# Kernel tuning notes

Hardware: AMD Instinct MI355X
Metric: run time of the kernel (lower is better)

## Reference

```python
import jax, jax.numpy as jnp
import numpy as np

EPS = 1e-5


def _ln(x, g, b):
    mu = jnp.mean(x, axis=-1, keepdims=True)
    var = jnp.var(x, axis=-1, keepdims=True)
    return (x - mu) * jax.lax.rsqrt(var + EPS) * g + b


def setup_inputs() -> dict:
    key = jax.random.key(0)
    ks = jax.random.split(key, 24)
    B, S, SD, PD, AD = 2, 512, 512, 128, 64
    H = PD * 2
    s = 0.02
    inp = {
        "sequence_input": jax.random.normal(ks[0], (B, S, SD), jnp.float32),
        "pair_input": jax.random.normal(ks[1], (B, S // 2, S // 2, PD), jnp.float32),
        # SequenceToPairBlock params
        "sn_g": jnp.ones((SD,), jnp.float32),
        "sn_b": jnp.zeros((SD,), jnp.float32),
        "Wq": jax.random.normal(ks[2], (SD, PD), jnp.float32) * s,
        "Wk": jax.random.normal(ks[3], (SD, PD), jnp.float32) * s,
        "Wyq": jax.random.normal(ks[4], (SD, PD), jnp.float32) * s,
        "Wyk": jax.random.normal(ks[5], (SD, PD), jnp.float32) * s,
        "Wdist": jax.random.normal(ks[6], (3, PD), jnp.float32) * s,
        "Wout": jax.random.normal(ks[7], (PD, PD), jnp.float32) * s,
        "bout": jnp.zeros((PD,), jnp.float32),
        # RowAttentionBlock params
        "rn_g": jnp.ones((PD,), jnp.float32),
        "rn_b": jnp.zeros((PD,), jnp.float32),
        "Wrq": jax.random.normal(ks[8], (PD, AD), jnp.float32) * s,
        "Wrk": jax.random.normal(ks[9], (PD, AD), jnp.float32) * s,
        "Wrv": jax.random.normal(ks[10], (PD, AD), jnp.float32) * s,
        "brv": jnp.zeros((AD,), jnp.float32),
        "Wro": jax.random.normal(ks[11], (AD, PD), jnp.float32) * s,
        "bro": jnp.zeros((PD,), jnp.float32),
        # PairMLPBlock params
        "mn_g": jnp.ones((PD,), jnp.float32),
        "mn_b": jnp.zeros((PD,), jnp.float32),
        "W1": jax.random.normal(ks[12], (PD, H), jnp.float32) * s,
        "b1": jnp.zeros((H,), jnp.float32),
        "W2": jax.random.normal(ks[13], (H, PD), jnp.float32) * s,
        "b2": jnp.zeros((PD,), jnp.float32),
    }
    return inp


def reference(sequence_input, pair_input, sn_g, sn_b, Wq, Wk, Wyq, Wyk, Wdist, Wout, bout,
              rn_g, rn_b, Wrq, Wrk, Wrv, brv, Wro, bro, mn_g, mn_b, W1, b1, W2, b2):
    # ---- SequenceToPairBlock ----
    x = _ln(sequence_input, sn_g, sn_b)               # [B,S,SD]
    B, S, SD = x.shape
    x = x.reshape(B, S // 2, 2, SD).mean(axis=2)       # avg_pool1d k=2,s=2 (S even) -> [B,P,SD]
    P = x.shape[1]
    q = x @ Wq                                         # [B,P,PD]
    k = x @ Wk
    pair_qk = q[:, :, None, :] + k[:, None, :, :]      # [B,P,P,PD]
    idx = jnp.arange(P, dtype=x.dtype)
    dist = idx[:, None] - idx[None, :]
    dist_scale = jnp.abs(dist) / max(1.0, float(P - 1))
    dist_feats = jnp.stack([dist_scale, jnp.sign(dist), jnp.exp(-dist_scale)], axis=-1)  # [P,P,3]
    pair_dist = dist_feats @ Wdist                     # [P,P,PD], broadcast over batch
    gx = jax.nn.gelu(x, approximate=False)
    yq = gx @ Wyq
    yk = gx @ Wyk
    pair_outer = yq[:, :, None, :] + yk[:, None, :, :]
    y = (pair_qk + pair_dist[None] + pair_outer) @ Wout + bout  # [B,P,P,PD]

    x = pair_input + y

    # ---- RowAttentionBlock (dropout off / eval) ----
    yn = _ln(x, rn_g, rn_b)
    qa = yn @ Wrq                                      # [B,P,P,AD]
    ka = yn @ Wrk
    va = yn @ Wrv + brv
    scale = 1.0 / jnp.sqrt(jnp.asarray(qa.shape[-1], x.dtype))
    logits = jnp.einsum('bird,bisd->birs', qa, ka) * scale
    attn = jax.nn.softmax(logits, axis=-1)
    o = jnp.einsum('birs,bisd->bird', attn, va)
    x = x + (o @ Wro + bro)

    # ---- PairMLPBlock ----
    h = _ln(x, mn_g, mn_b)
    x = x + (jax.nn.relu(h @ W1 + b1) @ W2 + b2)
    return x
```

## Files before the change

### kernel.cpp

```cpp
#include <hip/hip_runtime.h>
#include <hip/hip_bf16.h>

using bf16 = __hip_bfloat16;
typedef unsigned int uint;
typedef unsigned short ushort;
typedef __attribute__((ext_vector_type(8))) short bf16x8;
typedef __attribute__((ext_vector_type(4))) float f32x4;


__device__ __forceinline__ float bfraw(uint u) { return __uint_as_float(u << 16); }
__device__ __forceinline__ ushort f2bf(float f) {
    bf16 h = __float2bfloat16(f);
    return *reinterpret_cast<ushort*>(&h);
}
__device__ __forceinline__ float lbf(ushort u) { return __uint_as_float(((uint)u) << 16); }

#define MFMA_B16(a, b, c) __builtin_amdgcn_mfma_f32_16x16x32_bf16((a), (b), (c), 0, 0, 0)
#define LGKM0() asm volatile("s_waitcnt lgkmcnt(0)" ::: "memory")

__global__ __launch_bounds__(256) void k_ln_pool(
    const float* __restrict__ seq, const float* __restrict__ g,
    const float* __restrict__ be, float* __restrict__ x2)
{
    __shared__ float red[4][4];
    int bp = blockIdx.x;
    int t  = threadIdx.x;
    const float* r0 = seq + (size_t)(bp * 2) * 512;
    const float* r1 = r0 + 512;

    float a0 = r0[t], a1 = r0[t + 256];
    float c0 = r1[t], c1 = r1[t + 256];

    float s0 = a0 + a1, q0 = a0 * a0 + a1 * a1;
    float s1 = c0 + c1, q1 = c0 * c0 + c1 * c1;
#pragma unroll
    for (int off = 32; off; off >>= 1) {
        s0 += __shfl_xor(s0, off); q0 += __shfl_xor(q0, off);
        s1 += __shfl_xor(s1, off); q1 += __shfl_xor(q1, off);
    }
    int w = t >> 6, l = t & 63;
    if (l == 0) { red[0][w] = s0; red[1][w] = q0; red[2][w] = s1; red[3][w] = q1; }
    __syncthreads();
    s0 = red[0][0] + red[0][1] + red[0][2] + red[0][3];
    q0 = red[1][0] + red[1][1] + red[1][2] + red[1][3];
    s1 = red[2][0] + red[2][1] + red[2][2] + red[2][3];
    q1 = red[3][0] + red[3][1] + red[3][2] + red[3][3];

    const float inv = 1.0f / 512.0f;
    float mu0 = s0 * inv, var0 = q0 * inv - mu0 * mu0, rs0 = rsqrtf(var0 + 1e-5f);
    float mu1 = s1 * inv, var1 = q1 * inv - mu1 * mu1, rs1 = rsqrtf(var1 + 1e-5f);

    float g0 = g[t], g1 = g[t + 256];
    float e0 = be[t], e1 = be[t + 256];

    float o0 = 0.5f * ((a0 - mu0) * rs0 * g0 + e0 + (c0 - mu1) * rs1 * g0 + e0);
    float o1 = 0.5f * ((a1 - mu0) * rs0 * g1 + e1 + (c1 - mu1) * rs1 * g1 + e1);

    float* xo = x2 + (size_t)bp * 512;
    xo[t] = o0; xo[t + 256] = o1;
}

__global__ __launch_bounds__(128) void k_proj(
    const float* __restrict__ x2,
    const float* __restrict__ Wq, const float* __restrict__ Wk,
    const float* __restrict__ Wyq, const float* __restrict__ Wyk,
    const float* __restrict__ Wout, const float* __restrict__ bout,
    float* __restrict__ a2, float* __restrict__ c2)
{
    __shared__ float xr[512], gxr[512], ar[128], cr[128];
    int row = blockIdx.x;
    int t   = threadIdx.x;

    for (int u = t; u < 512; u += 128) {
        float v = x2[(size_t)row * 512 + u];
        xr[u]  = v;
        gxr[u] = 0.5f * v * (1.0f + erff(v * 0.70710678118654752f));
    }
    __syncthreads();

    float a = 0.f, c = 0.f;
    for (int s = 0; s < 512; s++) {
        float xs = xr[s], gs = gxr[s];
        a += xs * Wq[s * 128 + t] + gs * Wyq[s * 128 + t];
        c += xs * Wk[s * 128 + t] + gs * Wyk[s * 128 + t];
    }
    ar[t] = a; cr[t] = c;
    __syncthreads();

    float A = bout[t], C = 0.f;
    for (int u = 0; u < 128; u++) {
        float wv = Wout[u * 128 + t];
        A += ar[u] * wv;
        C += cr[u] * wv;
    }
    a2[(size_t)row * 128 + t] = A;
    c2[(size_t)row * 128 + t] = C;
}

__global__ __launch_bounds__(128) void k_wd2(
    const float* __restrict__ Wdist, const float* __restrict__ Wout,
    float* __restrict__ wd2)
{
    int t = threadIdx.x;
#pragma unroll
    for (int f = 0; f < 3; f++) {
        float acc = 0.f;
        for (int u = 0; u < 128; u++)
            acc += Wdist[f * 128 + u] * Wout[u * 128 + t];
        wd2[f * 128 + t] = acc;
    }
}

__global__ __launch_bounds__(512) void k_wt(
    const float* __restrict__ Wrq, const float* __restrict__ Wrk,
    const float* __restrict__ Wrv, const float* __restrict__ Wro,
    ushort* __restrict__ wqF, ushort* __restrict__ wkF,
    ushort* __restrict__ wvF, ushort* __restrict__ wroF)
{
    int idx = blockIdx.x * 512 + threadIdx.x;
    int m = idx >> 13;
    int o = idx & 8191;
    int f = o >> 9;
    int l = (o >> 3) & 63;
    int j = o & 7;
    if (m < 3) {
        int nt = f >> 2, kf = f & 3;
        const float* W = (m == 0) ? Wrq : (m == 1) ? Wrk : Wrv;
        ushort* T = (m == 0) ? wqF : (m == 1) ? wkF : wvF;
        T[o] = f2bf(W[(32 * kf + 8 * (l >> 4) + j) * 64 + 16 * nt + (l & 15)]);
    } else {
        int nt = f >> 1, kf2 = f & 1;
        wroF[o] = f2bf(Wro[(32 * kf2 + 8 * (l >> 4) + j) * 128 + 16 * nt + (l & 15)]);
    }
}

__global__ __launch_bounds__(512) void k_wt12(
    const float* __restrict__ W1, const float* __restrict__ W2,
    ushort* __restrict__ w1F, ushort* __restrict__ w2F)
{
    int idx = blockIdx.x * 512 + threadIdx.x;
    int o = idx & 32767;
    int f = o >> 9;
    int l = (o >> 3) & 63;
    int j = o & 7;
    int kb = f >> 5, nt = (f >> 2) & 7, kf = f & 3;
    if (idx < 32768) {
        int R = 128 * kb + 16 * nt + (l & 15);
        int C = 32 * kf + 8 * (l >> 4) + j;
        w1F[o] = f2bf(W1[C * 256 + R]);
    } else {
        int R2 = 16 * nt + (l & 15);
        int C2 = 128 * kb + 32 * kf + 8 * (l >> 4) + j;
        w2F[o] = f2bf(W2[C2 * 128 + R2]);
    }
}

__global__ __launch_bounds__(256) void k_assemble(
    const float* __restrict__ pair, const float* __restrict__ a2,
    const float* __restrict__ c2, const float* __restrict__ wd2,
    float* __restrict__ xout)
{
    size_t idx = (size_t)blockIdx.x * 256 + threadIdx.x;
    int d = (int)(idx & 127);
    size_t r = idx >> 7;
    int j = (int)(r & 255); r >>= 8;
    int i = (int)(r & 255);
    int b = (int)(r >> 8);

    float ds = fabsf((float)(i - j)) * (1.0f / 255.0f);
    float sg = (float)((i > j) - (i < j));
    float ex = __expf(-ds);

    float v = pair[idx]
            + a2[(size_t)(b * 256 + i) * 128 + d]
            + c2[(size_t)(b * 256 + j) * 128 + d]
            + ds * wd2[d] + sg * wd2[128 + d] + ex * wd2[256 + d];
    xout[idx] = v;
}

__global__ __launch_bounds__(64, 2) void k_qkv_asm(
    float* __restrict__ x, const float* __restrict__ pair,
    const float* __restrict__ a2, const float* __restrict__ c2,
    const float* __restrict__ wd2,
    const float* __restrict__ rn_g, const float* __restrict__ rn_b,
    const ushort* __restrict__ wqF, const ushort* __restrict__ wkF,
    const ushort* __restrict__ wvF, const float* __restrict__ brv,
    ushort* __restrict__ qA, ushort* __restrict__ kB, ushort* __restrict__ vB)
{
    __shared__ __align__(16) unsigned char smem[12288];
    int l = threadIdx.x;
    int g = l >> 4, lr = l & 15;
    int s = blockIdx.x & 511;
    int c = blockIdx.x >> 9;
    size_t xbase = (size_t)s * 32768 + (size_t)(32 * c) * 128;

    {
        float gl0 = rn_g[l], gl1 = rn_g[l + 64];
        float el0 = rn_b[l], el1 = rn_b[l + 64];
        int b  = s >> 8;
        int ii = s & 255;
        float a20 = a2[(size_t)s * 128 + l];
        float a21 = a2[(size_t)s * 128 + l + 64];
        float wdA0 = wd2[l],       wdA1 = wd2[l + 64];
        float wdB0 = wd2[128 + l], wdB1 = wd2[128 + l + 64];
        float wdC0 = wd2[256 + l], wdC1 = wd2[256 + l + 64];
#pragma unroll
        for (int bb = 0; bb < 8; bb++) {
            float p0[4], p1[4], c20[4], c21[4];
#pragma unroll
            for (int rr = 0; rr < 4; rr++) {
                size_t ro = xbase + (size_t)(4 * bb + rr) * 128;
                p0[rr] = pair[ro + l]; p1[rr] = pair[ro + l + 64];
                int j = 32 * c + 4 * bb + rr;
                c20[rr] = c2[(size_t)(b * 256 + j) * 128 + l];
                c21[rr] = c2[(size_t)(b * 256 + j) * 128 + l + 64];
            }
#pragma unroll
            for (int rr = 0; rr < 4; rr++) {
                int rloc = 4 * bb + rr;
                int j = 32 * c + rloc;
                float dsv = fabsf((float)(ii - j)) * (1.0f / 255.0f);
                float sgv = (float)((ii > j) - (ii < j));
                float exv = __expf(-dsv);
                float x0 = p0[rr] + a20 + c20[rr] + dsv * wdA0 + sgv * wdB0 + exv * wdC0;
                float x1 = p1[rr] + a21 + c21[rr] + dsv * wdA1 + sgv * wdB1 + exv * wdC1;
                size_t ro = xbase + (size_t)rloc * 128;
                x[ro + l] = x0; x[ro + l + 64] = x1;
                float sS = x0 + x1, qS = x0 * x0 + x1 * x1;
#pragma unroll
                for (int off = 32; off; off >>= 1) { sS += __shfl_xor(sS, off); qS += __shfl_xor(qS, off); }
                float mu = sS * (1.0f / 128.0f);
                float var = qS * (1.0f / 128.0f) - mu * mu;
                float rs = rsqrtf(var + 1e-5f);
                int sw = (rloc & 7) << 4;
                *(ushort*)(smem + rloc * 256 + ((2 * l) ^ sw))        = f2bf((x0 - mu) * rs * gl0 + el0);
                *(ushort*)(smem + rloc * 256 + ((2 * (l + 64)) ^ sw)) = f2bf((x1 - mu) * rs * gl1 + el1);
            }
        }
    }
    LGKM0();

    bf16x8 afr[2][4];
#pragma unroll
    for (int mt = 0; mt < 2; mt++)
#pragma unroll
        for (int kf = 0; kf < 4; kf++) {
            int row = 16 * mt + lr;
            afr[mt][kf] = *(const bf16x8*)(smem + row * 256 + ((16 * g + 64 * kf) ^ ((row & 7) << 4)));
        }

    unsigned char* dscr = smem + 8192;

#pragma unroll
    for (int mqk = 0; mqk < 2; mqk++) {
        const ushort* wF = mqk ? wkF : wqF;
        ushort* dst = mqk ? kB : qA;
        float scale = mqk ? 1.0f : 0.125f;
#pragma unroll
        for (int mt = 0; mt < 2; mt++) {
#pragma unroll
            for (int nt = 0; nt < 4; nt++) {
                f32x4 acc = (f32x4){0.f, 0.f, 0.f, 0.f};
#pragma unroll
                for (int kf = 0; kf < 4; kf++) {
                    bf16x8 bfr = *(const bf16x8*)(wF + (((nt << 2) | kf) << 9) + (l << 3));
                    acc = MFMA_B16(afr[mt][kf], bfr, acc);
                }
                int col = lr + 16 * nt;
#pragma unroll
                for (int i = 0; i < 4; i++) {
                    int row = 4 * g + i + 16 * mt;
                    int ad = row * 128 + ((2 * col) ^ ((row & 7) << 4));
                    *(ushort*)(dscr + ad) = f2bf(acc[i] * scale);
                }
            }
        }
        LGKM0();
#pragma unroll
        for (int mt = 0; mt < 2; mt++)
#pragma unroll
            for (int kf2 = 0; kf2 < 2; kf2++) {
                int row = 16 * mt + lr;
                int rd = row * 128 + ((64 * kf2 + 16 * g) ^ ((row & 7) << 4));
                bf16x8 v = *(const bf16x8*)(dscr + rd);
                *(bf16x8*)(dst + ((size_t)((s * 16 + 2 * c + mt) * 2 + kf2) << 9) + (l << 3)) = v;
            }
        LGKM0();
    }

#pragma unroll
    for (int mt = 0; mt < 2; mt++) {
#pragma unroll
        for (int nt = 0; nt < 4; nt++) {
            f32x4 acc = (f32x4){0.f, 0.f, 0.f, 0.f};
#pragma unroll
            for (int kf = 0; kf < 4; kf++) {
                bf16x8 bfr = *(const bf16x8*)(wvF + (((nt << 2) | kf) << 9) + (l << 3));
                acc = MFMA_B16(afr[mt][kf], bfr, acc);
            }
            int d = lr + 16 * nt;
            float bv = brv[d];
#pragma unroll
            for (int i = 0; i < 4; i++) {
                int kk = 4 * g + i + 16 * mt;
                int ad = d * 64 + ((2 * kk) ^ ((d & 3) << 4));
                *(ushort*)(dscr + ad) = f2bf(acc[i] + bv);
            }
        }
    }
    LGKM0();
#pragma unroll
    for (int nt2 = 0; nt2 < 4; nt2++) {
        int d = 16 * nt2 + lr;
        int rd = d * 64 + ((16 * g) ^ ((d & 3) << 4));
        bf16x8 vv = *(const bf16x8*)(dscr + rd);
        *(bf16x8*)(vB + ((size_t)((s * 4 + nt2) * 8 + c) << 9) + (l << 3)) = vv;
    }
}

__global__ __launch_bounds__(128, 2) void k_attn2(
    float* __restrict__ x,
    const ushort* __restrict__ qA, const ushort* __restrict__ kB,
    const ushort* __restrict__ vB, const ushort* __restrict__ wroF,
    const float* __restrict__ bro)
{
    __shared__ __align__(16) unsigned char smem_all[16384];
    int tid = threadIdx.x;
    int w = tid >> 6;
    int l = tid & 63, g = l >> 4, lr = l & 15;
    int s = blockIdx.x & 511;
    int qc = ((blockIdx.x >> 9) << 1) | w;
    unsigned char* smem = smem_all + (w << 13);

    bf16x8 qf[2][2];
#pragma unroll
    for (int mt = 0; mt < 2; mt++)
#pragma unroll
        for (int kf2 = 0; kf2 < 2; kf2++)
            qf[mt][kf2] = *(const bf16x8*)(qA + ((size_t)((s * 16 + 2 * qc + mt) * 2 + kf2) << 9) + (l << 3));

    float m_run[2][4], l_run[2][4];
    f32x4 oacc[2][4];
#pragma unroll
    for (int mt = 0; mt < 2; mt++)
#pragma unroll
        for (int i = 0; i < 4; i++) { m_run[mt][i] = -INFINITY; l_run[mt][i] = 0.f; }
#pragma unroll
    for (int mt = 0; mt < 2; mt++)
#pragma unroll
        for (int nt = 0; nt < 4; nt++) oacc[mt][nt] = (f32x4){0.f, 0.f, 0.f, 0.f};

    for (int t = 0; t < 2; t++) {
        f32x4 sacc[2][8];
#pragma unroll
        for (int mt = 0; mt < 2; mt++)
#pragma unroll
            for (int nt = 0; nt < 8; nt++) sacc[mt][nt] = (f32x4){0.f, 0.f, 0.f, 0.f};
#pragma unroll
        for (int nt = 0; nt < 8; nt++) {
            int kt = 8 * t + nt;
#pragma unroll
            for (int kf2 = 0; kf2 < 2; kf2++) {
                bf16x8 kfr = *(const bf16x8*)(kB + ((size_t)((s * 16 + kt) * 2 + kf2) << 9) + (l << 3));
                sacc[0][nt] = MFMA_B16(qf[0][kf2], kfr, sacc[0][nt]);
                sacc[1][nt] = MFMA_B16(qf[1][kf2], kfr, sacc[1][nt]);
            }
        }
#pragma unroll
        for (int mt = 0; mt < 2; mt++) {
#pragma unroll
            for (int i = 0; i < 4; i++) {
                float mx = sacc[mt][0][i];
#pragma unroll
                for (int nt = 1; nt < 8; nt++) mx = fmaxf(mx, sacc[mt][nt][i]);
#pragma unroll
                for (int off = 1; off < 16; off <<= 1) mx = fmaxf(mx, __shfl_xor(mx, off));
                float mnew = fmaxf(m_run[mt][i], mx);
                float corr = __expf(m_run[mt][i] - mnew);
                m_run[mt][i] = mnew;
                int row = 16 * mt + 4 * g + i;
                int swp = (row & 7) << 4;
                float rs = 0.f;
#pragma unroll
                for (int nt = 0; nt < 8; nt++) {
                    float p = __expf(sacc[mt][nt][i] - mnew);
                    rs += p;
                    int key = lr + 16 * nt;
                    *(ushort*)(smem + row * 256 + ((2 * key) ^ swp)) = f2bf(p);
                }
#pragma unroll
                for (int off = 1; off < 16; off <<= 1) rs += __shfl_xor(rs, off);
                l_run[mt][i] = l_run[mt][i] * corr + rs;
#pragma unroll
                for (int nt = 0; nt < 4; nt++) oacc[mt][nt][i] *= corr;
            }
        }
        LGKM0();
#pragma unroll
        for (int kc = 0; kc < 4; kc++) {
            bf16x8 pfr[2];
#pragma unroll
            for (int mt = 0; mt < 2; mt++) {
                int prow = 16 * mt + lr;
                pfr[mt] = *(const bf16x8*)(smem + prow * 256 + ((64 * kc + 16 * g) ^ ((prow & 7) << 4)));
            }
#pragma unroll
            for (int nt4 = 0; nt4 < 4; nt4++) {
                bf16x8 vfr = *(const bf16x8*)(vB + ((size_t)((s * 4 + nt4) * 8 + 4 * t + kc) << 9) + (l << 3));
                oacc[0][nt4] = MFMA_B16(pfr[0], vfr, oacc[0][nt4]);
                oacc[1][nt4] = MFMA_B16(pfr[1], vfr, oacc[1][nt4]);
            }
        }
        LGKM0();
    }

#pragma unroll
    for (int mt = 0; mt < 2; mt++)
#pragma unroll
        for (int i = 0; i < 4; i++) {
            float rl = 1.0f / l_run[mt][i];
            int row = 4 * g + i + 16 * mt;
            int swo = (row & 7) << 4;
#pragma unroll
            for (int nt = 0; nt < 4; nt++) {
                int col = lr + 16 * nt;
                *(ushort*)(smem + row * 128 + ((2 * col) ^ swo)) = f2bf(oacc[mt][nt][i] * rl);
            }
        }
    LGKM0();
    bf16x8 ofr[2][2];
#pragma unroll
    for (int mt = 0; mt < 2; mt++)
#pragma unroll
        for (int kf2 = 0; kf2 < 2; kf2++) {
            int row = 16 * mt + lr;
            int rd = row * 128 + ((64 * kf2 + 16 * g) ^ ((row & 7) << 4));
            ofr[mt][kf2] = *(const bf16x8*)(smem + rd);
        }
#pragma unroll
    for (int nt = 0; nt < 8; nt++) {
        f32x4 acc2[2];
        acc2[0] = (f32x4){0.f, 0.f, 0.f, 0.f};
        acc2[1] = (f32x4){0.f, 0.f, 0.f, 0.f};
#pragma unroll
        for (int kf2 = 0; kf2 < 2; kf2++) {
            bf16x8 wfr = *(const bf16x8*)(wroF + (((nt << 1) | kf2) << 9) + (l << 3));
            acc2[0] = MFMA_B16(ofr[0][kf2], wfr, acc2[0]);
            acc2[1] = MFMA_B16(ofr[1][kf2], wfr, acc2[1]);
        }
        int col = lr + 16 * nt;
        float brod = bro[col];
#pragma unroll
        for (int mt = 0; mt < 2; mt++)
#pragma unroll
            for (int i = 0; i < 4; i++) {
                int row = 32 * qc + 16 * mt + 4 * g + i;
                size_t off = (size_t)s * 32768 + (size_t)row * 128 + col;
                x[off] = x[off] + acc2[mt][i] + brod;
            }
    }
}

__global__ __launch_bounds__(512, 2) void k_attn_mfma(
    float* __restrict__ x,
    const float* __restrict__ rn_g, const float* __restrict__ rn_b,
    const ushort* __restrict__ wqF, const ushort* __restrict__ wkF,
    const ushort* __restrict__ wvF, const float* __restrict__ brv,
    const float* __restrict__ Wro, const float* __restrict__ bro)
{
    __shared__ __align__(16) unsigned char smem[131072];

    int tid = threadIdx.x;
    int w  = tid >> 6;
    int l  = tid & 63;
    int g  = l >> 4;
    int lr = l & 15;
    size_t base = (size_t)blockIdx.x * 32768;

    float gl0 = rn_g[l], gl1 = rn_g[l + 64];
    float el0 = rn_b[l], el1 = rn_b[l + 64];

    for (int h = 0; h < 2; h++) {
        for (int rr = 0; rr < 16; rr++) {
            int rloc = 16 * w + rr;
            size_t ro = base + (size_t)(128 * h + rloc) * 128;
            float x0 = x[ro + l], x1 = x[ro + l + 64];
            float s = x0 + x1, q = x0 * x0 + x1 * x1;
#pragma unroll
            for (int off = 32; off; off >>= 1) { s += __shfl_xor(s, off); q += __shfl_xor(q, off); }
            float mu = s * (1.0f / 128.0f);
            float var = q * (1.0f / 128.0f) - mu * mu;
            float rs = rsqrtf(var + 1e-5f);
            int sw = (rloc & 7) << 4;
            *(ushort*)(smem + 65536 + rloc * 256 + ((2 * l) ^ sw))        = f2bf((x0 - mu) * rs * gl0 + el0);
            *(ushort*)(smem + 65536 + rloc * 256 + ((2 * (l + 64)) ^ sw)) = f2bf((x1 - mu) * rs * gl1 + el1);
        }
        LGKM0();

        bf16x8 afr[4];
        int arow = 16 * w + lr;
#pragma unroll
        for (int kf = 0; kf < 4; kf++) {
            int ab = 65536 + arow * 256 + ((16 * g + 64 * kf) ^ ((arow & 7) << 4));
            afr[kf] = *(const bf16x8*)(smem + ab);
        }
#pragma unroll
        for (int m = 0; m < 3; m++) {
            const ushort* wT = (m == 0) ? wqF : (m == 1) ? wkF : wvF;
            f32x4 acc[4];
#pragma unroll
            for (int nt = 0; nt < 4; nt++) acc[nt] = (f32x4){0.f, 0.f, 0.f, 0.f};
#pragma unroll
            for (int kf = 0; kf < 4; kf++) {
#pragma unroll
                for (int nt = 0; nt < 4; nt++) {
                    bf16x8 bfr = *(const bf16x8*)(wT + (((nt << 2) | kf) << 9) + (l << 3));
                    acc[nt] = MFMA_B16(afr[kf], bfr, acc[nt]);
                }
            }
#pragma unroll
            for (int nt = 0; nt < 4; nt++) {
                int col = lr + 16 * nt;
                float bv = (m == 2) ? brv[col] : 0.f;
#pragma unroll
                for (int i = 0; i < 4; i++) {
                    int qrow = 128 * h + 16 * w + 4 * g + i;
                    float v = acc[nt][i];
                    if (m == 0) {
                        int ad = 98304 + qrow * 128 + ((2 * col) ^ ((qrow & 7) << 4));
                        *(ushort*)(smem + ad) = f2bf(v * 0.125f);
                    } else if (m == 1) {
                        int ad = qrow * 128 + ((2 * col) ^ ((qrow & 7) << 4));
                        *(ushort*)(smem + ad) = f2bf(v);
                    } else {
                        int ad = 32768 + col * 512 + ((2 * qrow) ^ ((col & 7) << 4));
                        *(ushort*)(smem + ad) = f2bf(v + bv);
                    }
                }
            }
        }
    }
    __syncthreads();

    bf16x8 qf[2][2];
#pragma unroll
    for (int mt = 0; mt < 2; mt++)
#pragma unroll
        for (int kf = 0; kf < 2; kf++) {
            int qrow = 32 * w + 16 * mt + lr;
            int ab = 98304 + qrow * 128 + ((16 * g + 64 * kf) ^ ((qrow & 7) << 4));
            qf[mt][kf] = *(const bf16x8*)(smem + ab);
        }
    __syncthreads();

    float m_run[2][4], l_run[2][4];
    f32x4 oacc[2][4];
#pragma unroll
    for (int mt = 0; mt < 2; mt++)
#pragma unroll
        for (int i = 0; i < 4; i++) { m_run[mt][i] = -INFINITY; l_run[mt][i] = 0.f; }
#pragma unroll
    for (int mt = 0; mt < 2; mt++)
#pragma unroll
        for (int nt = 0; nt < 4; nt++) oacc[mt][nt] = (f32x4){0.f, 0.f, 0.f, 0.f};

    for (int t = 0; t < 2; t++) {
        f32x4 sacc[2][8];
#pragma unroll
        for (int mt = 0; mt < 2; mt++)
#pragma unroll
            for (int nt = 0; nt < 8; nt++) sacc[mt][nt] = (f32x4){0.f, 0.f, 0.f, 0.f};
#pragma unroll
        for (int nt = 0; nt < 8; nt++) {
#pragma unroll
            for (int kf = 0; kf < 2; kf++) {
                int key = 128 * t + 16 * nt + lr;
                int ab = key * 128 + ((16 * g + 64 * kf) ^ ((key & 7) << 4));
                bf16x8 bfr = *(const bf16x8*)(smem + ab);
#pragma unroll
                for (int mt = 0; mt < 2; mt++)
                    sacc[mt][nt] = MFMA_B16(qf[mt][kf], bfr, sacc[mt][nt]);
            }
        }
#pragma unroll
        for (int mt = 0; mt < 2; mt++) {
#pragma unroll
            for (int i = 0; i < 4; i++) {
                float mx = sacc[mt][0][i];
#pragma unroll
                for (int nt = 1; nt < 8; nt++) mx = fmaxf(mx, sacc[mt][nt][i]);
#pragma unroll
                for (int off = 1; off < 16; off <<= 1) mx = fmaxf(mx, __shfl_xor(mx, off));
                float mnew = fmaxf(m_run[mt][i], mx);
                float corr = __expf(m_run[mt][i] - mnew);
                m_run[mt][i] = mnew;
                int qrow = 32 * w + 16 * mt + 4 * g + i;
                int swq = (qrow & 7) << 4;
                float rs = 0.f;
#pragma unroll
                for (int nt = 0; nt < 8; nt++) {
                    float p = __expf(sacc[mt][nt][i] - mnew);
                    rs += p;
                    int col = lr + 16 * nt;
                    *(ushort*)(smem + 65536 + qrow * 256 + ((2 * col) ^ swq)) = f2bf(p);
                }
#pragma unroll
                for (int off = 1; off < 16; off <<= 1) rs += __shfl_xor(rs, off);
                l_run[mt][i] = l_run[mt][i] * corr + rs;
#pragma unroll
                for (int nt = 0; nt < 4; nt++) oacc[mt][nt][i] *= corr;
            }
        }
        LGKM0();

#pragma unroll
        for (int kf = 0; kf < 4; kf++) {
            bf16x8 pfr[2];
#pragma unroll
            for (int mt = 0; mt < 2; mt++) {
                int qrow = 32 * w + 16 * mt + lr;
                int ab = 65536 + qrow * 256 + ((16 * g + 64 * kf) ^ ((qrow & 7) << 4));
                pfr[mt] = *(const bf16x8*)(smem + ab);
            }
#pragma unroll
            for (int nt = 0; nt < 4; nt++) {
                int d = lr + 16 * nt;
                int bb = 32768 + d * 512 + ((16 * g + 64 * kf + 256 * t) ^ ((d & 7) << 4));
                bf16x8 bfr = *(const bf16x8*)(smem + bb);
#pragma unroll
                for (int mt = 0; mt < 2; mt++)
                    oacc[mt][nt] = MFMA_B16(pfr[mt], bfr, oacc[mt][nt]);
            }
        }
    }
    __syncthreads();

#pragma unroll
    for (int mt = 0; mt < 2; mt++)
#pragma unroll
        for (int i = 0; i < 4; i++) {
            float rl = 1.0f / l_run[mt][i];
            int qrow = 32 * w + 16 * mt + 4 * g + i;
            int swq = (qrow & 7) << 4;
#pragma unroll
            for (int nt = 0; nt < 4; nt++) {
                int col = lr + 16 * nt;
                *(ushort*)(smem + 65536 + qrow * 128 + ((2 * col) ^ swq)) = f2bf(oacc[mt][nt][i] * rl);
            }
        }
    for (int e = tid; e < 8192; e += 512) {
        int k = e >> 7, c = e & 127;
        int ad = c * 128 + ((2 * k) ^ ((c & 7) << 4));
        *(ushort*)(smem + ad) = f2bf(Wro[e]);
    }
    __syncthreads();

#pragma unroll
    for (int mt = 0; mt < 2; mt++) {
        bf16x8 ofr[2];
#pragma unroll
        for (int kf = 0; kf < 2; kf++) {
            int orow = 32 * w + 16 * mt + lr;
            int ab = 65536 + orow * 128 + ((16 * g + 64 * kf) ^ ((orow & 7) << 4));
            ofr[kf] = *(const bf16x8*)(smem + ab);
        }
#pragma unroll
        for (int nt = 0; nt < 8; nt++) {
            f32x4 acc = (f32x4){0.f, 0.f, 0.f, 0.f};
#pragma unroll
            for (int kf = 0; kf < 2; kf++) {
                int c = lr + 16 * nt;
                int bb = c * 128 + ((16 * g + 64 * kf) ^ ((c & 7) << 4));
                bf16x8 bfr = *(const bf16x8*)(smem + bb);
                acc = MFMA_B16(ofr[kf], bfr, acc);
            }
            int col = lr + 16 * nt;
            float brod = bro[col];
#pragma unroll
            for (int i = 0; i < 4; i++) {
                int qrow = 32 * w + 16 * mt + 4 * g + i;
                size_t off = base + (size_t)qrow * 128 + col;
                x[off] = x[off] + acc[i] + brod;
            }
        }
    }
}

__global__ __launch_bounds__(64, 4) void k_mlp_mfma(
    float* __restrict__ x,
    const float* __restrict__ mn_g, const float* __restrict__ mn_b,
    const ushort* __restrict__ w1F, const ushort* __restrict__ w2F,
    const float* __restrict__ b1, const float* __restrict__ b2)
{
    __shared__ __align__(16) unsigned char smem[5120];
    int l = threadIdx.x;
    int g = l >> 4, lr = l & 15;
    size_t rbase = (size_t)blockIdx.x * 16;

    {
        float gl0 = mn_g[l], gl1 = mn_g[l + 64];
        float el0 = mn_b[l], el1 = mn_b[l + 64];
#pragma unroll
        for (int bb = 0; bb < 4; bb++) {
            float a0[4], a1[4];
#pragma unroll
            for (int rr = 0; rr < 4; rr++) {
                size_t ro = (rbase + 4 * bb + rr) * 128;
                a0[rr] = x[ro + l];
                a1[rr] = x[ro + l + 64];
            }
#pragma unroll
            for (int rr = 0; rr < 4; rr++) {
                int rloc = 4 * bb + rr;
                float x0 = a0[rr], x1 = a1[rr];
                float s = x0 + x1, q = x0 * x0 + x1 * x1;
#pragma unroll
                for (int off = 32; off; off >>= 1) { s += __shfl_xor(s, off); q += __shfl_xor(q, off); }
                float mu = s * (1.0f / 128.0f);
                float var = q * (1.0f / 128.0f) - mu * mu;
                float rs = rsqrtf(var + 1e-5f);
                int sw = (rloc & 7) << 4;
                *(ushort*)(smem + rloc * 256 + ((2 * l) ^ sw))        = f2bf((x0 - mu) * rs * gl0 + el0);
                *(ushort*)(smem + rloc * 256 + ((2 * (l + 64)) ^ sw)) = f2bf((x1 - mu) * rs * gl1 + el1);
            }
        }
    }
    LGKM0();

    bf16x8 afr[4];
#pragma unroll
    for (int kf = 0; kf < 4; kf++) {
        afr[kf] = *(const bf16x8*)(smem + lr * 256 + ((16 * g + 64 * kf) ^ ((lr & 7) << 4)));
    }

    f32x4 oacc[8];
#pragma unroll
    for (int nt = 0; nt < 8; nt++) oacc[nt] = (f32x4){0.f, 0.f, 0.f, 0.f};

#pragma unroll
    for (int kb = 0; kb < 2; kb++) {
#pragma unroll
        for (int cc = 0; cc < 4; cc++) {
#pragma unroll
            for (int nt2 = 0; nt2 < 2; nt2++) {
                int nt = 2 * cc + nt2;
                f32x4 acc = (f32x4){0.f, 0.f, 0.f, 0.f};
#pragma unroll
                for (int kf = 0; kf < 4; kf++) {
                    bf16x8 bfr = *(const bf16x8*)(w1F + (((((kb << 3) | nt) << 2) | kf) << 9) + (l << 3));
                    acc = MFMA_B16(afr[kf], bfr, acc);
                }
                float bb1 = b1[128 * kb + 16 * nt + lr];
                int colc = lr + 16 * nt2;
#pragma unroll
                for (int i = 0; i < 4; i++) {
                    int row = 4 * g + i;
                    int ad = 4096 + row * 64 + ((2 * colc) ^ ((row & 3) << 4));
                    *(ushort*)(smem + ad) = f2bf(fmaxf(acc[i] + bb1, 0.f));
                }
            }
            LGKM0();

            bf16x8 hfr = *(const bf16x8*)(smem + 4096 + lr * 64 + ((16 * g) ^ ((lr & 3) << 4)));
#pragma unroll
            for (int nt = 0; nt < 8; nt++) {
                bf16x8 bfr = *(const bf16x8*)(w2F + (((((kb << 3) | nt) << 2) | cc) << 9) + (l << 3));
                oacc[nt] = MFMA_B16(hfr, bfr, oacc[nt]);
            }
            LGKM0();
        }
    }

#pragma unroll
    for (int nt = 0; nt < 8; nt++) {
        int col = 16 * nt + lr;
#pragma unroll
        for (int i = 0; i < 4; i++) {
            int row = 4 * g + i;
            int ad = row * 256 + ((2 * col) ^ ((row & 7) << 4));
            *(ushort*)(smem + ad) = f2bf(oacc[nt][i]);
        }
    }
    LGKM0();
    {
        float b20 = b2[l], b21 = b2[l + 64];
#pragma unroll
        for (int rr = 0; rr < 16; rr++) {
            int sw = (rr & 7) << 4;
            float d0 = lbf(*(const ushort*)(smem + rr * 256 + ((2 * l) ^ sw)));
            float d1 = lbf(*(const ushort*)(smem + rr * 256 + ((2 * (l + 64)) ^ sw)));
            size_t ro = (rbase + rr) * 128;
            x[ro + l]      = x[ro + l]      + d0 + b20;
            x[ro + l + 64] = x[ro + l + 64] + d1 + b21;
        }
    }
}

extern "C" void kernel_launch(void* const* d_in, const int* in_sizes, int n_in,
                              void* d_out, int out_size, void* d_ws, size_t ws_size,
                              hipStream_t stream)
{
    const float* seq   = (const float*)d_in[0];
    const float* pair  = (const float*)d_in[1];
    const float* sn_g  = (const float*)d_in[2];
    const float* sn_b  = (const float*)d_in[3];
    const float* Wq    = (const float*)d_in[4];
    const float* Wk    = (const float*)d_in[5];
    const float* Wyq   = (const float*)d_in[6];
    const float* Wyk   = (const float*)d_in[7];
    const float* Wdist = (const float*)d_in[8];
    const float* Wout  = (const float*)d_in[9];
    const float* bout  = (const float*)d_in[10];
    const float* rn_g  = (const float*)d_in[11];
    const float* rn_b  = (const float*)d_in[12];
    const float* Wrq   = (const float*)d_in[13];
    const float* Wrk   = (const float*)d_in[14];
    const float* Wrv   = (const float*)d_in[15];
    const float* brv   = (const float*)d_in[16];
    const float* Wro   = (const float*)d_in[17];
    const float* bro   = (const float*)d_in[18];
    const float* mn_g  = (const float*)d_in[19];
    const float* mn_b  = (const float*)d_in[20];
    const float* W1    = (const float*)d_in[21];
    const float* b1    = (const float*)d_in[22];
    const float* W2    = (const float*)d_in[23];
    const float* b2    = (const float*)d_in[24];
    (void)in_sizes; (void)n_in; (void)out_size;

    float*  x2   = (float*)d_ws;
    float*  a2   = x2 + 262144;
    float*  c2   = a2 + 65536;
    float*  wd2  = c2 + 65536;
    ushort* wqF  = (ushort*)(wd2 + 512);
    ushort* wkF  = wqF + 8192;
    ushort* wvF  = wkF + 8192;
    ushort* wroF = wvF + 8192;
    ushort* w1F  = wroF + 8192;
    ushort* w2F  = w1F + 32768;
    ushort* qA   = w2F + 32768;
    ushort* kBp  = qA + 8388608;
    ushort* vBp  = kBp + 8388608;
    float*  xres = (float*)d_out;

    const size_t WS_NEED_SPLIT = 52103168ull;
    bool use_split = (ws_size >= WS_NEED_SPLIT);

    k_ln_pool  <<<512,   256, 0, stream>>>(seq, sn_g, sn_b, x2);
    k_proj     <<<512,   128, 0, stream>>>(x2, Wq, Wk, Wyq, Wyk, Wout, bout, a2, c2);
    k_wd2      <<<1,     128, 0, stream>>>(Wdist, Wout, wd2);
    k_wt       <<<64,    512, 0, stream>>>(Wrq, Wrk, Wrv, Wro, wqF, wkF, wvF, wroF);
    k_wt12     <<<128,   512, 0, stream>>>(W1, W2, w1F, w2F);
    if (use_split) {
        k_qkv_asm<<<4096, 64,  0, stream>>>(xres, pair, a2, c2, wd2,
                                            rn_g, rn_b, wqF, wkF, wvF, brv,
                                            qA, kBp, vBp);
        k_attn2  <<<2048, 128, 0, stream>>>(xres, qA, kBp, vBp, wroF, bro);
    } else {
        k_assemble <<<65536, 256, 0, stream>>>(pair, a2, c2, wd2, xres);
        k_attn_mfma<<<512,   512, 0, stream>>>(xres, rn_g, rn_b, wqF, wkF, wvF, brv, Wro, bro);
    }
    k_mlp_mfma <<<8192,  64,  0, stream>>>(xres, mn_g, mn_b, w1F, w2F, b1, b2);
}
```

Measured before the change: 209.4 us.

## Fuse pair MLP block into row-attention output kernel

```diff
diff --git a/kernel.cpp b/kernel.cpp
--- a/kernel.cpp
+++ b/kernel.cpp
@@ -318,19 +318,22 @@
     }
 }
 
-__global__ __launch_bounds__(128, 2) void k_attn2(
+__global__ __launch_bounds__(128, 2) void k_attn_mlp(
     float* __restrict__ x,
     const ushort* __restrict__ qA, const ushort* __restrict__ kB,
     const ushort* __restrict__ vB, const ushort* __restrict__ wroF,
-    const float* __restrict__ bro)
-{
-    __shared__ __align__(16) unsigned char smem_all[16384];
+    const float* __restrict__ bro,
+    const float* __restrict__ mn_g, const float* __restrict__ mn_b,
+    const ushort* __restrict__ w1F, const ushort* __restrict__ w2F,
+    const float* __restrict__ b1, const float* __restrict__ b2)
+{
+    __shared__ __align__(16) unsigned char smem_all[20480];
     int tid = threadIdx.x;
     int w = tid >> 6;
     int l = tid & 63, g = l >> 4, lr = l & 15;
     int s = blockIdx.x & 511;
     int qc = ((blockIdx.x >> 9) << 1) | w;
-    unsigned char* smem = smem_all + (w << 13);
+    unsigned char* smem = smem_all + w * 10240;
 
     bf16x8 qf[2][2];
 #pragma unroll
@@ -437,6 +440,8 @@
             int rd = row * 128 + ((64 * kf2 + 16 * g) ^ ((row & 7) << 4));
             ofr[mt][kf2] = *(const bf16x8*)(smem + rd);
         }
+
+    f32x4 xn[2][8];
 #pragma unroll
     for (int nt = 0; nt < 8; nt++) {
         f32x4 acc2[2];
@@ -456,7 +461,110 @@
             for (int i = 0; i < 4; i++) {
                 int row = 32 * qc + 16 * mt + 4 * g + i;
                 size_t off = (size_t)s * 32768 + (size_t)row * 128 + col;
-                x[off] = x[off] + acc2[mt][i] + brod;
+                xn[mt][nt][i] = x[off] + acc2[mt][i] + brod;
+            }
+    }
+
+    {
+        float glc[8], elc[8];
+#pragma unroll
+        for (int nt = 0; nt < 8; nt++) { glc[nt] = mn_g[lr + 16 * nt]; elc[nt] = mn_b[lr + 16 * nt]; }
+#pragma unroll
+        for (int mt = 0; mt < 2; mt++)
+#pragma unroll
+            for (int i = 0; i < 4; i++) {
+                float sS = 0.f, qS = 0.f;
+#pragma unroll
+                for (int nt = 0; nt < 8; nt++) { float v = xn[mt][nt][i]; sS += v; qS += v * v; }
+#pragma unroll
+                for (int off = 1; off < 16; off <<= 1) { sS += __shfl_xor(sS, off); qS += __shfl_xor(qS, off); }
+                float mu = sS * (1.0f / 128.0f);
+                float var = qS * (1.0f / 128.0f) - mu * mu;
+                float rs = rsqrtf(var + 1e-5f);
+                int row = 16 * mt + 4 * g + i;
+                int sw = (row & 7) << 4;
+#pragma unroll
+                for (int nt = 0; nt < 8; nt++) {
+                    int col = lr + 16 * nt;
+                    *(ushort*)(smem + row * 256 + ((2 * col) ^ sw)) =
+                        f2bf((xn[mt][nt][i] - mu) * rs * glc[nt] + elc[nt]);
+                }
+            }
+    }
+    LGKM0();
+
+    bf16x8 afrm[2][4];
+#pragma unroll
+    for (int mt = 0; mt < 2; mt++)
+#pragma unroll
+        for (int kf = 0; kf < 4; kf++) {
+            int row = 16 * mt + lr;
+            afrm[mt][kf] = *(const bf16x8*)(smem + row * 256 + ((16 * g + 64 * kf) ^ ((row & 7) << 4)));
+        }
+
+    f32x4 mo[2][8];
+#pragma unroll
+    for (int mt = 0; mt < 2; mt++)
+#pragma unroll
+        for (int nt = 0; nt < 8; nt++) mo[mt][nt] = (f32x4){0.f, 0.f, 0.f, 0.f};
+
+    unsigned char* hsc = smem + 8192;
+#pragma unroll
+    for (int kb = 0; kb < 2; kb++) {
+#pragma unroll
+        for (int cc = 0; cc < 4; cc++) {
+#pragma unroll
+            for (int nt2 = 0; nt2 < 2; nt2++) {
+                int nt = 2 * cc + nt2;
+                f32x4 a1[2];
+                a1[0] = (f32x4){0.f, 0.f, 0.f, 0.f};
+                a1[1] = (f32x4){0.f, 0.f, 0.f, 0.f};
+#pragma unroll
+                for (int kf = 0; kf < 4; kf++) {
+                    bf16x8 bfr = *(const bf16x8*)(w1F + (((((kb << 3) | nt) << 2) | kf) << 9) + (l << 3));
+                    a1[0] = MFMA_B16(afrm[0][kf], bfr, a1[0]);
+                    a1[1] = MFMA_B16(afrm[1][kf], bfr, a1[1]);
+                }
+                float bb1 = b1[128 * kb + 16 * nt + lr];
+                int colc = lr + 16 * nt2;
+#pragma unroll
+                for (int mt = 0; mt < 2; mt++)
+#pragma unroll
+                    for (int i = 0; i < 4; i++) {
+                        int row = 16 * mt + 4 * g + i;
+                        int ad = row * 64 + ((2 * colc) ^ ((row & 3) << 4));
+                        *(ushort*)(hsc + ad) = f2bf(fmaxf(a1[mt][i] + bb1, 0.f));
+                    }
+            }
+            LGKM0();
+
+            bf16x8 hfr[2];
+#pragma unroll
+            for (int mt = 0; mt < 2; mt++) {
+                int row = 16 * mt + lr;
+                hfr[mt] = *(const bf16x8*)(hsc + row * 64 + ((16 * g) ^ ((row & 3) << 4)));
+            }
+#pragma unroll
+            for (int nt = 0; nt < 8; nt++) {
+                bf16x8 bfr = *(const bf16x8*)(w2F + (((((kb << 3) | nt) << 2) | cc) << 9) + (l << 3));
+                mo[0][nt] = MFMA_B16(hfr[0], bfr, mo[0][nt]);
+                mo[1][nt] = MFMA_B16(hfr[1], bfr, mo[1][nt]);
+            }
+            LGKM0();
+        }
+    }
+
+#pragma unroll
+    for (int nt = 0; nt < 8; nt++) {
+        int col = lr + 16 * nt;
+        float b2c = b2[col];
+#pragma unroll
+        for (int mt = 0; mt < 2; mt++)
+#pragma unroll
+            for (int i = 0; i < 4; i++) {
+                int row = 32 * qc + 16 * mt + 4 * g + i;
+                size_t off = (size_t)s * 32768 + (size_t)row * 128 + col;
+                x[off] = xn[mt][nt][i] + mo[mt][nt][i] + b2c;
             }
     }
 }
@@ -851,13 +959,14 @@
     k_wt       <<<64,    512, 0, stream>>>(Wrq, Wrk, Wrv, Wro, wqF, wkF, wvF, wroF);
     k_wt12     <<<128,   512, 0, stream>>>(W1, W2, w1F, w2F);
     if (use_split) {
-        k_qkv_asm<<<4096, 64,  0, stream>>>(xres, pair, a2, c2, wd2,
-                                            rn_g, rn_b, wqF, wkF, wvF, brv,
-                                            qA, kBp, vBp);
-        k_attn2  <<<2048, 128, 0, stream>>>(xres, qA, kBp, vBp, wroF, bro);
+        k_qkv_asm <<<4096, 64,  0, stream>>>(xres, pair, a2, c2, wd2,
+                                             rn_g, rn_b, wqF, wkF, wvF, brv,
+                                             qA, kBp, vBp);
+        k_attn_mlp<<<2048, 128, 0, stream>>>(xres, qA, kBp, vBp, wroF, bro,
+                                             mn_g, mn_b, w1F, w2F, b1, b2);
     } else {
         k_assemble <<<65536, 256, 0, stream>>>(pair, a2, c2, wd2, xres);
         k_attn_mfma<<<512,   512, 0, stream>>>(xres, rn_g, rn_b, wqF, wkF, wvF, brv, Wro, bro);
-    }
-    k_mlp_mfma <<<8192,  64,  0, stream>>>(xres, mn_g, mn_b, w1F, w2F, b1, b2);
-}
+        k_mlp_mfma <<<8192,  64,  0, stream>>>(xres, mn_g, mn_b, w1F, w2F, b1, b2);
+    }
+}
```

Result: slower. 284.3 us (+35.8%).
